# Kernel optimization log

Hardware: AMD Instinct MI355X
Metric: run time of the kernel (lower is better)

The kernel has to match this reference:

```python
import jax, jax.numpy as jnp
import numpy as np

SUPPORT = 10
NEIGHBOR_NUM = 20
DEGREE = 8
NEG_SLOPE = 0.2
EPS = 1e-12


def _norm(x, axis):
    n = jnp.linalg.norm(x, axis=axis, keepdims=True)
    return x / jnp.maximum(n, EPS)


def knn_index(v, k):
    # v: (b, n, 3) -> (b, n, k) indices of k nearest (self excluded)
    inner = jnp.einsum('bnd,bmd->bnm', v, v)
    quad = jnp.sum(v * v, axis=2)
    dist = quad[:, :, None] - 2.0 * inner + quad[:, None, :]
    _, idx = jax.lax.top_k(-dist, k + 1)  # smallest distances
    return idx[:, :, 1:]


def gather_nb(feat, idx):
    # feat (b,n,c), idx (b,n,k) -> (b,n,k,c)
    b = feat.shape[0]
    return feat[jnp.arange(b)[:, None, None], idx]


def nb_dir_norm(vertices, idx):
    nb = gather_nb(vertices, idx) - vertices[:, :, None, :]
    return _norm(nb, axis=-1)


def op3d(idx, vertices, directions, kernel_num):
    # Conv_surface: directions (3, support*kernel)
    ndn = nb_dir_norm(vertices, idx)                 # (b,n,k,3)
    sdn = _norm(directions, axis=0)
    theta = jax.nn.relu(jnp.einsum('bnkd,de->bnke', ndn, sdn))
    b, n, kk, _ = theta.shape
    theta = theta.reshape(b, n, kk, SUPPORT, kernel_num)
    return jnp.sum(jnp.max(theta, axis=2), axis=2)    # (b,n,kernel)


def opnd(idx, vertices, feat, w, bias, directions, out_ch):
    # Conv_layer: w (in,(s+1)*out), bias ((s+1)*out), directions (3, s*out)
    ndn = nb_dir_norm(vertices, idx)
    sdn = _norm(directions, axis=0)
    theta = jax.nn.relu(jnp.einsum('bnkd,de->bnke', ndn, sdn))  # (b,n,k,s*out)
    fo = feat @ w + bias                                        # (b,n,(s+1)*out)
    fc = fo[:, :, :out_ch]
    fs = gather_nb(fo[:, :, out_ch:], idx)                      # (b,n,k,s*out)
    b, n, kk, _ = theta.shape
    act = (theta * fs).reshape(b, n, kk, SUPPORT, out_ch)
    return fc + jnp.sum(jnp.max(act, axis=2), axis=2)


def tree_gcn(x, w_root, w_branch, w_l1, w_l2, bias, activation):
    # depth-0 upsampling TreeGCN: x (b,node,in) -> (b,node*DEGREE,out)
    b, node, in_f = x.shape
    root = x @ w_root                                           # (b,node,out)
    br = jax.nn.leaky_relu(jnp.einsum('bni,nij->bnj', x, w_branch), NEG_SLOPE)
    br = br.reshape(b, node * DEGREE, in_f)
    br = (br @ w_l1) @ w_l2                                     # (b,node*deg,out)
    out = jnp.repeat(root, DEGREE, axis=1) + br
    if activation:
        out = jax.nn.leaky_relu(out + jnp.tile(bias, (1, node, 1)), NEG_SLOPE)
    return out


def setup_inputs() -> dict:
    key = jax.random.key(0)
    ks = iter(jax.random.split(key, 32))
    r = lambda shape: (jax.random.normal(next(ks), shape, dtype=jnp.float32) * 0.1)
    inp = {
        'coase_points': jax.random.normal(next(ks), (2, 512, 3), dtype=jnp.float32),
        'd0': r((3, SUPPORT * 32)),
        'w1': r((32, (SUPPORT + 1) * 64)), 'b1': r(((SUPPORT + 1) * 64,)), 'dir1': r((3, SUPPORT * 64)),
        'd2': r((3, SUPPORT * 32)),
        'w3': r((32, (SUPPORT + 1) * 64)), 'b3': r(((SUPPORT + 1) * 64,)), 'dir3': r((3, SUPPORT * 64)),
        'w4': r((64, (SUPPORT + 1) * 64)), 'b4': r(((SUPPORT + 1) * 64,)), 'dir4': r((3, SUPPORT * 64)),
        'w5': r((64, (SUPPORT + 1) * 64)), 'b5': r(((SUPPORT + 1) * 64,)), 'dir5': r((3, SUPPORT * 64)),
        'root1': r((64, 3)), 'branch1': r((512, 64, DEGREE * 64)),
        'loop1a': r((64, 64 * SUPPORT)), 'loop1b': r((64 * SUPPORT, 3)), 'bias1': r((1, DEGREE, 3)),
        'root2': r((64, 3)), 'branch2': r((4096, 64, DEGREE * 64)),
        'loop2a': r((64, 64 * SUPPORT)), 'loop2b': r((64 * SUPPORT, 3)),
    }
    return inp


def reference(coase_points, d0, w1, b1, dir1, d2, w3, b3, dir3, w4, b4, dir4,
              w5, b5, dir5, root1, branch1, loop1a, loop1b, bias1,
              root2, branch2, loop2a, loop2b):
    idx = knn_index(coase_points, NEIGHBOR_NUM)
    fm0 = jax.nn.relu(op3d(idx, coase_points, d0, 32))  # dropout is identity in eval
    fm1 = jax.nn.relu(opnd(idx, coase_points, fm0, w1, b1, dir1, 64))
    pc1 = tree_gcn(fm1, root1, branch1, loop1a, loop1b, bias1, True)   # (b, 4096, 3)
    idx2 = knn_index(pc1, NEIGHBOR_NUM)
    fm2 = jax.nn.relu(op3d(idx2, pc1, d2, 32))
    fm3 = jax.nn.relu(opnd(idx2, pc1, fm2, w3, b3, dir3, 64))
    fm4 = jax.nn.relu(opnd(idx2, pc1, fm3, w4, b4, dir4, 64))
    fm5 = jax.nn.relu(opnd(idx2, pc1, fm4, w5, b5, dir5, 64))
    pc2 = tree_gcn(fm5, root2, branch2, loop2a, loop2b, None, False)   # (b, 32768, 3)
    return pc1, pc2
```

## Files before the change

kernel.cpp:

```cpp
#include <hip/hip_runtime.h>
#include <hip/hip_bf16.h>
#include <stdint.h>

#define SUPPORT 10
#define KNN 20
#define DEGREE 8

__global__ __launch_bounds__(256) void prep_kernel(
    const float* __restrict__ d0, const float* __restrict__ dir1,
    const float* __restrict__ d2, const float* __restrict__ dir3,
    const float* __restrict__ dir4, const float* __restrict__ dir5,
    float* __restrict__ sdn0, float* __restrict__ sdn1, float* __restrict__ sdn2,
    float* __restrict__ sdn3, float* __restrict__ sdn4, float* __restrict__ sdn5,
    const float* __restrict__ l1a, const float* __restrict__ l1b,
    const float* __restrict__ l2a, const float* __restrict__ l2b,
    float* __restrict__ wc1, float* __restrict__ wc2,
    const float* __restrict__ pts1,
    float* __restrict__ px1, float* __restrict__ py1, float* __restrict__ pz1) {
#pragma clang fp contract(off)
  if (blockIdx.x < 13) {
    int t = blockIdx.x * 256 + threadIdx.x;
    if (t >= 3200) return;
    const float* src; float* dst; int cols; int e;
    if (t < 320)       { src = d0;   dst = sdn0; cols = 320; e = t; }
    else if (t < 960)  { src = dir1; dst = sdn1; cols = 640; e = t - 320; }
    else if (t < 1280) { src = d2;   dst = sdn2; cols = 320; e = t - 960; }
    else if (t < 1920) { src = dir3; dst = sdn3; cols = 640; e = t - 1280; }
    else if (t < 2560) { src = dir4; dst = sdn4; cols = 640; e = t - 1920; }
    else               { src = dir5; dst = sdn5; cols = 640; e = t - 2560; }
    float a = src[e], b = src[cols + e], c = src[2 * cols + e];
    float nrm = sqrtf(a * a + b * b + c * c);
    nrm = fmaxf(nrm, 1e-12f);
    dst[e] = a / nrm; dst[cols + e] = b / nrm; dst[2 * cols + e] = c / nrm;
  } else if (blockIdx.x < 15) {
    int which = blockIdx.x - 13;
    int tt = threadIdx.x;
    if (tt >= 192) return;
    const float* A  = which ? l2a : l1a;
    const float* Bm = which ? l2b : l1b;
    float* out = which ? wc2 : wc1;
    int i = tt / 3, c = tt % 3;
    float s = 0.f;
    for (int k = 0; k < 640; ++k) s = fmaf(A[i * 640 + k], Bm[k * 3 + c], s);
    out[i * 3 + c] = s;
  } else {
    int t = (blockIdx.x - 15) * 256 + threadIdx.x;
    if (t >= 1024) return;
    px1[t] = pts1[t * 3];
    py1[t] = pts1[t * 3 + 1];
    pz1[t] = pts1[t * 3 + 2];
  }
}

__global__ __launch_bounds__(256) void soa2_kernel(const float* __restrict__ pc1,
                                                   float* __restrict__ px,
                                                   float* __restrict__ py,
                                                   float* __restrict__ pz) {
  int t = blockIdx.x * 256 + threadIdx.x;
  if (t >= 8192) return;
  px[t] = pc1[t * 3];
  py[t] = pc1[t * 3 + 1];
  pz[t] = pc1[t * 3 + 2];
}

template <int MPER, int WAVES>
__global__ __launch_bounds__(WAVES * 64) void knn_kernel(
    const float* __restrict__ px, const float* __restrict__ py,
    const float* __restrict__ pz, int N, int* __restrict__ idx_out) {
#pragma clang fp contract(off)
  extern __shared__ uint32_t kbuf[];
  int w = threadIdx.x >> 6, lane = threadIdx.x & 63;
  int g = blockIdx.x * WAVES + w;
  int b = g / N, n = g % N;
  volatile uint32_t* K = kbuf + (size_t)w * 64 * MPER;
  const float* PX = px + (size_t)b * N;
  const float* PY = py + (size_t)b * N;
  const float* PZ = pz + (size_t)b * N;

  float nx = PX[n], ny = PY[n], nz = PZ[n];
  float qn = nx * nx + ny * ny + nz * nz;

  unsigned long long mymin = ~0ull;
  for (int j = 0; j < MPER; ++j) {
    int m = j * 64 + lane;
    float mx = PX[m], my = PY[m], mz = PZ[m];
    float inner = nx * mx + ny * my + nz * mz;
    float qm = mx * mx + my * my + mz * mz;
    float d = (qn - 2.0f * inner) + qm;
    uint32_t u = __float_as_uint(d);
    u ^= (u & 0x80000000u) ? 0xFFFFFFFFu : 0x80000000u;
    K[lane * MPER + (j ^ (lane & (MPER - 1)))] = u;
    unsigned long long key = ((unsigned long long)u << 32) | (unsigned)m;
    mymin = key < mymin ? key : mymin;
  }
  for (int r = 0; r < 21; ++r) {
    unsigned long long best = mymin;
#pragma unroll
    for (int s = 1; s < 64; s <<= 1) {
      unsigned long long o = __shfl_xor(best, s, 64);
      best = o < best ? o : best;
    }
    unsigned m = (unsigned)best;
    if (r > 0 && lane == 0) idx_out[(size_t)g * KNN + (r - 1)] = (int)m;
    if (r == 20) break;
    int owner = m & 63, slot = m >> 6;
    if (lane == slot) K[owner * MPER + (slot ^ (owner & (MPER - 1)))] = 0xFFFFFFFFu;
    unsigned long long cand = ~0ull;
    if (lane < MPER) {
      uint32_t v = K[owner * MPER + (lane ^ (owner & (MPER - 1)))];
      cand = ((unsigned long long)v << 32) | (unsigned)(lane * 64 + owner);
    }
#pragma unroll
    for (int s = 1; s < 64; s <<= 1) {
      unsigned long long o = __shfl_xor(cand, s, 64);
      cand = o < cand ? o : cand;
    }
    if (lane == owner) mymin = cand;
  }
}

__global__ __launch_bounds__(256) void ndn_kernel(const float* __restrict__ pts,
                                                  const int* __restrict__ idx,
                                                  float* __restrict__ ndn, int N) {
#pragma clang fp contract(off)
  int t = blockIdx.x * 256 + threadIdx.x;
  int total = 2 * N * KNN;
  if (t >= total) return;
  int k = t % KNN, g = t / KNN;
  int b = g / N, n = g % N;
  int m = idx[(size_t)g * KNN + k];
  const float* pb = pts + (size_t)b * N * 3;
  float dx = pb[m * 3] - pb[n * 3];
  float dy = pb[m * 3 + 1] - pb[n * 3 + 1];
  float dz = pb[m * 3 + 2] - pb[n * 3 + 2];
  float nr = sqrtf(dx * dx + dy * dy + dz * dz);
  nr = fmaxf(nr, 1e-12f);
  ndn[(size_t)t * 3] = dx / nr; ndn[(size_t)t * 3 + 1] = dy / nr; ndn[(size_t)t * 3 + 2] = dz / nr;
}

__global__ __launch_bounds__(256) void op3d_kernel(const float* __restrict__ ndn,
                                                   const float* __restrict__ sdn,
                                                   float* __restrict__ out, int N) {
#pragma clang fp contract(off)
  int c = threadIdx.x & 31;
  int g = (blockIdx.x * 256 + threadIdx.x) >> 5;
  if (g >= 2 * N) return;
  const float* nd = ndn + (size_t)g * 60;
  float sv0[SUPPORT], sv1[SUPPORT], sv2[SUPPORT], mm[SUPPORT];
#pragma unroll
  for (int s = 0; s < SUPPORT; ++s) {
    sv0[s] = sdn[s * 32 + c];
    sv1[s] = sdn[320 + s * 32 + c];
    sv2[s] = sdn[640 + s * 32 + c];
    mm[s] = 0.f;
  }
  for (int k = 0; k < KNN; ++k) {
    float nx = nd[k * 3], ny = nd[k * 3 + 1], nz = nd[k * 3 + 2];
#pragma unroll
    for (int s = 0; s < SUPPORT; ++s) {
      float t = nx * sv0[s] + ny * sv1[s] + nz * sv2[s];
      mm[s] = fmaxf(mm[s], t);
    }
  }
  float acc = 0.f;
#pragma unroll
  for (int s = 0; s < SUPPORT; ++s) acc += mm[s];
  out[(size_t)g * 32 + c] = acc;
}

template <int K>
__global__ __launch_bounds__(256) void fo_kernel(const float* __restrict__ feat,
                                                 const float* __restrict__ wmat,
                                                 const float* __restrict__ bias,
                                                 float* __restrict__ fo, int N) {
  __shared__ float fL[8 * K];
  int t = threadIdx.x;
  int gbase = blockIdx.x * 8;
  for (int i = t; i < 8 * K; i += 256) fL[i] = feat[(size_t)gbase * K + i];
  __syncthreads();
  float a0[8], a1[8], a2[8];
#pragma unroll
  for (int gg = 0; gg < 8; ++gg) { a0[gg] = 0.f; a1[gg] = 0.f; a2[gg] = 0.f; }
  bool has3 = (t < 192);
  for (int i = 0; i < K; ++i) {
    float w0 = wmat[i * 704 + t];
    float w1 = wmat[i * 704 + t + 256];
    float w2 = has3 ? wmat[i * 704 + t + 512] : 0.f;
#pragma unroll
    for (int gg = 0; gg < 8; ++gg) {
      float f = fL[gg * K + i];
      a0[gg] = fmaf(f, w0, a0[gg]);
      a1[gg] = fmaf(f, w1, a1[gg]);
      a2[gg] = fmaf(f, w2, a2[gg]);
    }
  }
  float b0 = bias[t], b1 = bias[t + 256], b2 = has3 ? bias[t + 512] : 0.f;
#pragma unroll
  for (int gg = 0; gg < 8; ++gg) {
    size_t base = (size_t)(gbase + gg) * 704;
    fo[base + t] = a0[gg] + b0;
    fo[base + t + 256] = a1[gg] + b1;
    if (has3) fo[base + t + 512] = a2[gg] + b2;
  }
}

__global__ __launch_bounds__(256) void opnd_kernel(const float* __restrict__ ndn,
                                                   const int* __restrict__ idx,
                                                   const float* __restrict__ fo,
                                                   const float* __restrict__ sdn,
                                                   float* __restrict__ fm, int N) {
#pragma clang fp contract(off)
  __shared__ float ndL[4][64];
  __shared__ int offL[4][24];
  int nb = gridDim.x;
  int lb = (blockIdx.x & 7) * (nb >> 3) + (blockIdx.x >> 3);
  int w = threadIdx.x >> 6, lane = threadIdx.x & 63;
  int g = lb * 4 + w;
  if (lane < 60) ndL[w][lane] = ndn[(size_t)g * 60 + lane];
  if (lane < KNN) offL[w][lane] = ((g / N) * N + idx[(size_t)g * KNN + lane]) * 704 + 64;
  __syncthreads();
  const float* ndw = ndL[w];
  const int* offw = offL[w];
  float sv0[SUPPORT], sv1[SUPPORT], sv2[SUPPORT], mm[SUPPORT];
#pragma unroll
  for (int s = 0; s < SUPPORT; ++s) {
    sv0[s] = sdn[s * 64 + lane];
    sv1[s] = sdn[640 + s * 64 + lane];
    sv2[s] = sdn[1280 + s * 64 + lane];
    mm[s] = -__builtin_inff();
  }
  for (int k = 0; k < KNN; ++k) {
    float nx = ndw[k * 3], ny = ndw[k * 3 + 1], nz = ndw[k * 3 + 2];
    int off = offw[k];
#pragma unroll
    for (int s = 0; s < SUPPORT; ++s) {
      float t = fmaxf(nx * sv0[s] + ny * sv1[s] + nz * sv2[s], 0.f);
      float f = fo[(size_t)off + s * 64 + lane];
      mm[s] = fmaxf(mm[s], t * f);
    }
  }
  float acc = 0.f;
#pragma unroll
  for (int s = 0; s < SUPPORT; ++s) acc += mm[s];
  float fc = fo[(size_t)g * 704 + lane];
  float v = fc + acc;
  fm[(size_t)g * 64 + lane] = fmaxf(v, 0.f);
}

__global__ __launch_bounds__(256) void tree_exact_kernel(
    const float* __restrict__ x, const float* __restrict__ wroot,
    const float* __restrict__ wb, const float* __restrict__ l1,
    const float* __restrict__ l2, const float* __restrict__ bias,
    float* __restrict__ out, int node) {
#pragma clang fp contract(off)
  __shared__ float xL[2][64];
  __shared__ float brL[2][512];
  __shared__ float tL[16][640];
  __shared__ float rootv[2][3];
  int n = blockIdx.x, t = threadIdx.x;
  if (t < 128) xL[t >> 6][t & 63] = x[(size_t)(t >> 6) * node * 64 + (size_t)n * 64 + (t & 63)];
  __syncthreads();
  {
    const float* wrow = wb + (size_t)n * 64 * 512;
    int j0 = 2 * t;
    float a00 = 0.f, a01 = 0.f, a10 = 0.f, a11 = 0.f;
    for (int i = 0; i < 64; ++i) {
      float w0 = wrow[(size_t)i * 512 + j0];
      float w1 = wrow[(size_t)i * 512 + j0 + 1];
      float f0 = xL[0][i], f1 = xL[1][i];
      a00 = a00 + f0 * w0; a01 = a01 + f0 * w1;
      a10 = a10 + f1 * w0; a11 = a11 + f1 * w1;
    }
    brL[0][j0]     = a00 >= 0.f ? a00 : 0.2f * a00;
    brL[0][j0 + 1] = a01 >= 0.f ? a01 : 0.2f * a01;
    brL[1][j0]     = a10 >= 0.f ? a10 : 0.2f * a10;
    brL[1][j0 + 1] = a11 >= 0.f ? a11 : 0.2f * a11;
  }
  if (t < 6) {
    int b = t / 3, c = t % 3;
    float r = 0.f;
    for (int i = 0; i < 64; ++i) r = fmaf(xL[b][i], wroot[i * 3 + c], r);
    rootv[b][c] = r;
  }
  __syncthreads();
#pragma unroll 4
  for (int u = 0; u < 40; ++u) {
    int e = u * 256 + t;
    int p = e / 640, j = e % 640;
    const float* brow = brL[p >> 3] + (p & 7) * 64;
    float acc = 0.f;
    for (int i = 0; i < 64; ++i)
      acc = fmaf(brow[i], l1[i * 640 + j], acc);
    tL[p][j] = acc;
  }
  __syncthreads();
  if (t < 48) {
    int p = t / 3, c = t % 3, b = p >> 3, d = p & 7;
    float s = 0.f;
    for (int j = 0; j < 640; ++j) s = fmaf(tL[p][j], l2[j * 3 + c], s);
    float v = rootv[b][c] + s;
    v = v + bias[d * 3 + c];
    v = v >= 0.f ? v : 0.2f * v;
    out[((size_t)b * node * DEGREE + (size_t)n * DEGREE + d) * 3 + c] = v;
  }
}

__global__ __launch_bounds__(256) void tree_kernel(const float* __restrict__ x,
                                                   const float* __restrict__ wroot,
                                                   const float* __restrict__ wb,
                                                   const float* __restrict__ wc,
                                                   float* __restrict__ out,
                                                   int node) {
  __shared__ float xL[2][2][64];
  __shared__ float brL[2][2][512];
  int t = threadIdx.x;
  int n0 = blockIdx.x * 2;
  if (t < 256) {
    int which = t >> 6;
    int ns = which >> 1, bb = which & 1;
    xL[ns][bb][t & 63] = x[(size_t)bb * node * 64 + (size_t)(n0 + ns) * 64 + (t & 63)];
  }
  __syncthreads();
  int ns = t >> 7;
  int j0 = (t & 127) * 4;
  const float* wrow = wb + (size_t)(n0 + ns) * 64 * 512;
  float a0x = 0.f, a0y = 0.f, a0z = 0.f, a0w = 0.f;
  float a1x = 0.f, a1y = 0.f, a1z = 0.f, a1w = 0.f;
  for (int i = 0; i < 64; ++i) {
    float4 wv = *(const float4*)(wrow + (size_t)i * 512 + j0);
    float f0 = xL[ns][0][i], f1 = xL[ns][1][i];
    a0x += f0 * wv.x; a0y += f0 * wv.y; a0z += f0 * wv.z; a0w += f0 * wv.w;
    a1x += f1 * wv.x; a1y += f1 * wv.y; a1z += f1 * wv.z; a1w += f1 * wv.w;
  }
  brL[ns][0][j0]     = a0x >= 0.f ? a0x : 0.2f * a0x;
  brL[ns][0][j0 + 1] = a0y >= 0.f ? a0y : 0.2f * a0y;
  brL[ns][0][j0 + 2] = a0z >= 0.f ? a0z : 0.2f * a0z;
  brL[ns][0][j0 + 3] = a0w >= 0.f ? a0w : 0.2f * a0w;
  brL[ns][1][j0]     = a1x >= 0.f ? a1x : 0.2f * a1x;
  brL[ns][1][j0 + 1] = a1y >= 0.f ? a1y : 0.2f * a1y;
  brL[ns][1][j0 + 2] = a1z >= 0.f ? a1z : 0.2f * a1z;
  brL[ns][1][j0 + 3] = a1w >= 0.f ? a1w : 0.2f * a1w;
  __syncthreads();
  if (t < 96) {
    int nsub = t / 48, rem = t % 48;
    int b = rem / 24, r2 = rem % 24, d = r2 / 3, c = r2 % 3;
    float root = 0.f, brs = 0.f;
    for (int i = 0; i < 64; ++i) {
      root = fmaf(xL[nsub][b][i], wroot[i * 3 + c], root);
      brs  = fmaf(brL[nsub][b][d * 64 + i], wc[i * 3 + c], brs);
    }
    float v = root + brs;
    out[((size_t)b * node * DEGREE + (size_t)(n0 + nsub) * DEGREE + d) * 3 + c] = v;
  }
}

extern "C" void kernel_launch(void* const* d_in, const int* in_sizes, int n_in,
                              void* d_out, int out_size, void* d_ws, size_t ws_size,
                              hipStream_t stream) {
  const float* pts1    = (const float*)d_in[0];
  const float* d0      = (const float*)d_in[1];
  const float* w1      = (const float*)d_in[2];
  const float* b1      = (const float*)d_in[3];
  const float* dir1    = (const float*)d_in[4];
  const float* d2      = (const float*)d_in[5];
  const float* w3      = (const float*)d_in[6];
  const float* b3      = (const float*)d_in[7];
  const float* dir3    = (const float*)d_in[8];
  const float* w4      = (const float*)d_in[9];
  const float* b4      = (const float*)d_in[10];
  const float* dir4    = (const float*)d_in[11];
  const float* w5      = (const float*)d_in[12];
  const float* b5      = (const float*)d_in[13];
  const float* dir5    = (const float*)d_in[14];
  const float* root1   = (const float*)d_in[15];
  const float* branch1 = (const float*)d_in[16];
  const float* l1a     = (const float*)d_in[17];
  const float* l1b     = (const float*)d_in[18];
  const float* bias1   = (const float*)d_in[19];
  const float* root2   = (const float*)d_in[20];
  const float* branch2 = (const float*)d_in[21];
  const float* l2a     = (const float*)d_in[22];
  const float* l2b     = (const float*)d_in[23];

  float* ws = (float*)d_ws;
  size_t o = 0;
  float* sdn0 = ws + o; o += 960;
  float* sdn1 = ws + o; o += 1920;
  float* sdn2 = ws + o; o += 960;
  float* sdn3 = ws + o; o += 1920;
  float* sdn4 = ws + o; o += 1920;
  float* sdn5 = ws + o; o += 1920;
  float* wc1  = ws + o; o += 192;
  float* wc2  = ws + o; o += 192;
  float* px1  = ws + o; o += 1024;
  float* py1  = ws + o; o += 1024;
  float* pz1  = ws + o; o += 1024;
  float* px2  = ws + o; o += 8192;
  float* py2  = ws + o; o += 8192;
  float* pz2  = ws + o; o += 8192;
  int*   idxb = (int*)(ws + o); o += (size_t)2 * 4096 * KNN;
  float* ndnb = ws + o; o += (size_t)2 * 4096 * KNN * 3;
  float* fo   = ws + o; o += (size_t)2 * 4096 * 704;
  float* fmA  = ws + o; o += (size_t)2 * 4096 * 64;
  float* fmB  = ws + o; o += (size_t)2 * 4096 * 64;

  float* pc1 = (float*)d_out;
  float* pc2 = (float*)d_out + 2 * 4096 * 3;

  prep_kernel<<<19, 256, 0, stream>>>(d0, dir1, d2, dir3, dir4, dir5,
                                      sdn0, sdn1, sdn2, sdn3, sdn4, sdn5,
                                      l1a, l1b, l2a, l2b, wc1, wc2,
                                      pts1, px1, py1, pz1);

  knn_kernel<8, 4><<<2 * 512 / 4, 256, 4 * 64 * 8 * 4, stream>>>(px1, py1, pz1, 512, idxb);
  ndn_kernel<<<(2 * 512 * KNN + 255) / 256, 256, 0, stream>>>(pts1, idxb, ndnb, 512);
  op3d_kernel<<<2 * 512 * 32 / 256, 256, 0, stream>>>(ndnb, sdn0, fmA, 512);
  fo_kernel<32><<<2 * 512 / 8, 256, 0, stream>>>(fmA, w1, b1, fo, 512);
  opnd_kernel<<<2 * 512 / 4, 256, 0, stream>>>(ndnb, idxb, fo, sdn1, fmB, 512);
  tree_exact_kernel<<<512, 256, 0, stream>>>(fmB, root1, branch1, l1a, l1b,
                                             bias1, pc1, 512);

  soa2_kernel<<<32, 256, 0, stream>>>(pc1, px2, py2, pz2);
  knn_kernel<64, 2><<<2 * 4096 / 2, 128, 2 * 64 * 64 * 4, stream>>>(px2, py2, pz2, 4096, idxb);
  ndn_kernel<<<(2 * 4096 * KNN + 255) / 256, 256, 0, stream>>>(pc1, idxb, ndnb, 4096);
  op3d_kernel<<<2 * 4096 * 32 / 256, 256, 0, stream>>>(ndnb, sdn2, fmA, 4096);
  fo_kernel<32><<<2 * 4096 / 8, 256, 0, stream>>>(fmA, w3, b3, fo, 4096);
  opnd_kernel<<<2 * 4096 / 4, 256, 0, stream>>>(ndnb, idxb, fo, sdn3, fmB, 4096);
  fo_kernel<64><<<2 * 4096 / 8, 256, 0, stream>>>(fmB, w4, b4, fo, 4096);
  opnd_kernel<<<2 * 4096 / 4, 256, 0, stream>>>(ndnb, idxb, fo, sdn4, fmA, 4096);
  fo_kernel<64><<<2 * 4096 / 8, 256, 0, stream>>>(fmA, w5, b5, fo, 4096);
  opnd_kernel<<<2 * 4096 / 4, 256, 0, stream>>>(ndnb, idxb, fo, sdn5, fmB, 4096);
  tree_kernel<<<4096 / 2, 256, 0, stream>>>(fmB, root2, branch2, wc2, pc2, 4096);
}
```

Baseline: 655.3 us.

## Fuse neighbor-direction into kNN, op3d into fo, and SoA split into tree kernel

The kNN kernel now keeps the selected neighbor index in a per-lane register and, once selection ends, writes the indices and the normalized neighbor direction vectors directly. This removes the separate ndn kernel. op3d and the first feature matmul are merged into one kernel that keeps op3d output in shared memory. The first tree kernel also writes SoA coordinates, so the soa2 kernel is gone. The aim is fewer launches and less global round-tripping, at the cost of extra register and work load in the kNN and op3dfo kernels.

```diff
diff --git a/kernel.cpp b/kernel.cpp
--- a/kernel.cpp
+++ b/kernel.cpp
@@ -52,21 +52,11 @@
   }
 }
 
-__global__ __launch_bounds__(256) void soa2_kernel(const float* __restrict__ pc1,
-                                                   float* __restrict__ px,
-                                                   float* __restrict__ py,
-                                                   float* __restrict__ pz) {
-  int t = blockIdx.x * 256 + threadIdx.x;
-  if (t >= 8192) return;
-  px[t] = pc1[t * 3];
-  py[t] = pc1[t * 3 + 1];
-  pz[t] = pc1[t * 3 + 2];
-}
-
 template <int MPER, int WAVES>
 __global__ __launch_bounds__(WAVES * 64) void knn_kernel(
     const float* __restrict__ px, const float* __restrict__ py,
-    const float* __restrict__ pz, int N, int* __restrict__ idx_out) {
+    const float* __restrict__ pz, int N, int* __restrict__ idx_out,
+    float* __restrict__ ndn) {
 #pragma clang fp contract(off)
   extern __shared__ uint32_t kbuf[];
   int w = threadIdx.x >> 6, lane = threadIdx.x & 63;
@@ -93,6 +83,7 @@
     unsigned long long key = ((unsigned long long)u << 32) | (unsigned)m;
     mymin = key < mymin ? key : mymin;
   }
+  unsigned pick = 0;
   for (int r = 0; r < 21; ++r) {
     unsigned long long best = mymin;
 #pragma unroll
@@ -101,7 +92,7 @@
       best = o < best ? o : best;
     }
     unsigned m = (unsigned)best;
-    if (r > 0 && lane == 0) idx_out[(size_t)g * KNN + (r - 1)] = (int)m;
+    if (r > 0 && lane == r - 1) pick = m;
     if (r == 20) break;
     int owner = m & 63, slot = m >> 6;
     if (lane == slot) K[owner * MPER + (slot ^ (owner & (MPER - 1)))] = 0xFFFFFFFFu;
@@ -117,78 +108,100 @@
     }
     if (lane == owner) mymin = cand;
   }
-}
-
-__global__ __launch_bounds__(256) void ndn_kernel(const float* __restrict__ pts,
-                                                  const int* __restrict__ idx,
-                                                  float* __restrict__ ndn, int N) {
+  if (lane < KNN) {
+    idx_out[(size_t)g * KNN + lane] = (int)pick;
+    float mx = PX[pick], my = PY[pick], mz = PZ[pick];
+    float dx = mx - nx, dy = my - ny, dz = mz - nz;
+    float nr = sqrtf(dx * dx + dy * dy + dz * dz);
+    nr = fmaxf(nr, 1e-12f);
+    size_t base = (size_t)g * 60 + (size_t)lane * 3;
+    ndn[base] = dx / nr; ndn[base + 1] = dy / nr; ndn[base + 2] = dz / nr;
+  }
+}
+
+__global__ __launch_bounds__(256) void op3dfo_kernel(const float* __restrict__ ndn,
+                                                     const float* __restrict__ sdn,
+                                                     const float* __restrict__ wmat,
+                                                     const float* __restrict__ bias,
+                                                     float* __restrict__ fo, int N) {
 #pragma clang fp contract(off)
-  int t = blockIdx.x * 256 + threadIdx.x;
-  int total = 2 * N * KNN;
-  if (t >= total) return;
-  int k = t % KNN, g = t / KNN;
-  int b = g / N, n = g % N;
-  int m = idx[(size_t)g * KNN + k];
-  const float* pb = pts + (size_t)b * N * 3;
-  float dx = pb[m * 3] - pb[n * 3];
-  float dy = pb[m * 3 + 1] - pb[n * 3 + 1];
-  float dz = pb[m * 3 + 2] - pb[n * 3 + 2];
-  float nr = sqrtf(dx * dx + dy * dy + dz * dz);
-  nr = fmaxf(nr, 1e-12f);
-  ndn[(size_t)t * 3] = dx / nr; ndn[(size_t)t * 3 + 1] = dy / nr; ndn[(size_t)t * 3 + 2] = dz / nr;
-}
-
-__global__ __launch_bounds__(256) void op3d_kernel(const float* __restrict__ ndn,
-                                                   const float* __restrict__ sdn,
-                                                   float* __restrict__ out, int N) {
-#pragma clang fp contract(off)
-  int c = threadIdx.x & 31;
-  int g = (blockIdx.x * 256 + threadIdx.x) >> 5;
-  if (g >= 2 * N) return;
-  const float* nd = ndn + (size_t)g * 60;
-  float sv0[SUPPORT], sv1[SUPPORT], sv2[SUPPORT], mm[SUPPORT];
-#pragma unroll
-  for (int s = 0; s < SUPPORT; ++s) {
-    sv0[s] = sdn[s * 32 + c];
-    sv1[s] = sdn[320 + s * 32 + c];
-    sv2[s] = sdn[640 + s * 32 + c];
-    mm[s] = 0.f;
-  }
-  for (int k = 0; k < KNN; ++k) {
-    float nx = nd[k * 3], ny = nd[k * 3 + 1], nz = nd[k * 3 + 2];
+  __shared__ float ndL[8 * 60];
+  __shared__ float fL[8 * 32];
+  int t = threadIdx.x;
+  int gbase = blockIdx.x * 8;
+  for (int i = t; i < 8 * 60; i += 256) ndL[i] = ndn[(size_t)gbase * 60 + i];
+  __syncthreads();
+  {
+    int gg = t >> 5, c = t & 31;
+    const float* nd = ndL + gg * 60;
+    float sv0[SUPPORT], sv1[SUPPORT], sv2[SUPPORT], mm[SUPPORT];
 #pragma unroll
     for (int s = 0; s < SUPPORT; ++s) {
-      float t = nx * sv0[s] + ny * sv1[s] + nz * sv2[s];
-      mm[s] = fmaxf(mm[s], t);
-    }
-  }
-  float acc = 0.f;
-#pragma unroll
-  for (int s = 0; s < SUPPORT; ++s) acc += mm[s];
-  out[(size_t)g * 32 + c] = acc;
-}
-
-template <int K>
+      sv0[s] = sdn[s * 32 + c];
+      sv1[s] = sdn[320 + s * 32 + c];
+      sv2[s] = sdn[640 + s * 32 + c];
+      mm[s] = 0.f;
+    }
+    for (int k = 0; k < KNN; ++k) {
+      float nx = nd[k * 3], ny = nd[k * 3 + 1], nz = nd[k * 3 + 2];
+#pragma unroll
+      for (int s = 0; s < SUPPORT; ++s) {
+        float th = nx * sv0[s] + ny * sv1[s] + nz * sv2[s];
+        mm[s] = fmaxf(mm[s], th);
+      }
+    }
+    float acc = 0.f;
+#pragma unroll
+    for (int s = 0; s < SUPPORT; ++s) acc += mm[s];
+    fL[gg * 32 + c] = acc;
+  }
+  __syncthreads();
+  float a0[8], a1[8], a2[8];
+#pragma unroll
+  for (int gg = 0; gg < 8; ++gg) { a0[gg] = 0.f; a1[gg] = 0.f; a2[gg] = 0.f; }
+  bool has3 = (t < 192);
+  for (int i = 0; i < 32; ++i) {
+    float w0 = wmat[i * 704 + t];
+    float w1 = wmat[i * 704 + t + 256];
+    float w2 = has3 ? wmat[i * 704 + t + 512] : 0.f;
+#pragma unroll
+    for (int gg = 0; gg < 8; ++gg) {
+      float f = fL[gg * 32 + i];
+      a0[gg] = fmaf(f, w0, a0[gg]);
+      a1[gg] = fmaf(f, w1, a1[gg]);
+      a2[gg] = fmaf(f, w2, a2[gg]);
+    }
+  }
+  float b0 = bias[t], b1 = bias[t + 256], b2 = has3 ? bias[t + 512] : 0.f;
+#pragma unroll
+  for (int gg = 0; gg < 8; ++gg) {
+    size_t base = (size_t)(gbase + gg) * 704;
+    fo[base + t] = a0[gg] + b0;
+    fo[base + t + 256] = a1[gg] + b1;
+    if (has3) fo[base + t + 512] = a2[gg] + b2;
+  }
+}
+
 __global__ __launch_bounds__(256) void fo_kernel(const float* __restrict__ feat,
                                                  const float* __restrict__ wmat,
                                                  const float* __restrict__ bias,
                                                  float* __restrict__ fo, int N) {
-  __shared__ float fL[8 * K];
+  __shared__ float fL[8 * 64];
   int t = threadIdx.x;
   int gbase = blockIdx.x * 8;
-  for (int i = t; i < 8 * K; i += 256) fL[i] = feat[(size_t)gbase * K + i];
+  for (int i = t; i < 8 * 64; i += 256) fL[i] = feat[(size_t)gbase * 64 + i];
   __syncthreads();
   float a0[8], a1[8], a2[8];
 #pragma unroll
   for (int gg = 0; gg < 8; ++gg) { a0[gg] = 0.f; a1[gg] = 0.f; a2[gg] = 0.f; }
   bool has3 = (t < 192);
-  for (int i = 0; i < K; ++i) {
+  for (int i = 0; i < 64; ++i) {
     float w0 = wmat[i * 704 + t];
     float w1 = wmat[i * 704 + t + 256];
     float w2 = has3 ? wmat[i * 704 + t + 512] : 0.f;
 #pragma unroll
     for (int gg = 0; gg < 8; ++gg) {
-      float f = fL[gg * K + i];
+      float f = fL[gg * 64 + i];
       a0[gg] = fmaf(f, w0, a0[gg]);
       a1[gg] = fmaf(f, w1, a1[gg]);
       a2[gg] = fmaf(f, w2, a2[gg]);
@@ -251,7 +264,8 @@
     const float* __restrict__ x, const float* __restrict__ wroot,
     const float* __restrict__ wb, const float* __restrict__ l1,
     const float* __restrict__ l2, const float* __restrict__ bias,
-    float* __restrict__ out, int node) {
+    float* __restrict__ out, int node,
+    float* __restrict__ px2, float* __restrict__ py2, float* __restrict__ pz2) {
 #pragma clang fp contract(off)
   __shared__ float xL[2][64];
   __shared__ float brL[2][512];
@@ -302,6 +316,8 @@
     v = v + bias[d * 3 + c];
     v = v >= 0.f ? v : 0.2f * v;
     out[((size_t)b * node * DEGREE + (size_t)n * DEGREE + d) * 3 + c] = v;
+    int p2 = b * node * DEGREE + n * DEGREE + d;
+    if (c == 0) px2[p2] = v; else if (c == 1) py2[p2] = v; else pz2[p2] = v;
   }
 }
 
@@ -315,7 +331,7 @@
   __shared__ float brL[2][2][512];
   int t = threadIdx.x;
   int n0 = blockIdx.x * 2;
-  if (t < 256) {
+  {
     int which = t >> 6;
     int ns = which >> 1, bb = which & 1;
     xL[ns][bb][t & 63] = x[(size_t)bb * node * 64 + (size_t)(n0 + ns) * 64 + (t & 63)];
@@ -412,23 +428,18 @@
                                       l1a, l1b, l2a, l2b, wc1, wc2,
                                       pts1, px1, py1, pz1);
 
-  knn_kernel<8, 4><<<2 * 512 / 4, 256, 4 * 64 * 8 * 4, stream>>>(px1, py1, pz1, 512, idxb);
-  ndn_kernel<<<(2 * 512 * KNN + 255) / 256, 256, 0, stream>>>(pts1, idxb, ndnb, 512);
-  op3d_kernel<<<2 * 512 * 32 / 256, 256, 0, stream>>>(ndnb, sdn0, fmA, 512);
-  fo_kernel<32><<<2 * 512 / 8, 256, 0, stream>>>(fmA, w1, b1, fo, 512);
+  knn_kernel<8, 4><<<2 * 512 / 4, 256, 4 * 64 * 8 * 4, stream>>>(px1, py1, pz1, 512, idxb, ndnb);
+  op3dfo_kernel<<<2 * 512 / 8, 256, 0, stream>>>(ndnb, sdn0, w1, b1, fo, 512);
   opnd_kernel<<<2 * 512 / 4, 256, 0, stream>>>(ndnb, idxb, fo, sdn1, fmB, 512);
   tree_exact_kernel<<<512, 256, 0, stream>>>(fmB, root1, branch1, l1a, l1b,
-                                             bias1, pc1, 512);
-
-  soa2_kernel<<<32, 256, 0, stream>>>(pc1, px2, py2, pz2);
-  knn_kernel<64, 2><<<2 * 4096 / 2, 128, 2 * 64 * 64 * 4, stream>>>(px2, py2, pz2, 4096, idxb);
-  ndn_kernel<<<(2 * 4096 * KNN + 255) / 256, 256, 0, stream>>>(pc1, idxb, ndnb, 4096);
-  op3d_kernel<<<2 * 4096 * 32 / 256, 256, 0, stream>>>(ndnb, sdn2, fmA, 4096);
-  fo_kernel<32><<<2 * 4096 / 8, 256, 0, stream>>>(fmA, w3, b3, fo, 4096);
+                                             bias1, pc1, 512, px2, py2, pz2);
+
+  knn_kernel<64, 2><<<2 * 4096 / 2, 128, 2 * 64 * 64 * 4, stream>>>(px2, py2, pz2, 4096, idxb, ndnb);
+  op3dfo_kernel<<<2 * 4096 / 8, 256, 0, stream>>>(ndnb, sdn2, w3, b3, fo, 4096);
   opnd_kernel<<<2 * 4096 / 4, 256, 0, stream>>>(ndnb, idxb, fo, sdn3, fmB, 4096);
-  fo_kernel<64><<<2 * 4096 / 8, 256, 0, stream>>>(fmB, w4, b4, fo, 4096);
+  fo_kernel<<<2 * 4096 / 8, 256, 0, stream>>>(fmB, w4, b4, fo, 4096);
   opnd_kernel<<<2 * 4096 / 4, 256, 0, stream>>>(ndnb, idxb, fo, sdn4, fmA, 4096);
-  fo_kernel<64><<<2 * 4096 / 8, 256, 0, stream>>>(fmA, w5, b5, fo, 4096);
+  fo_kernel<<<2 * 4096 / 8, 256, 0, stream>>>(fmA, w5, b5, fo, 4096);
   opnd_kernel<<<2 * 4096 / 4, 256, 0, stream>>>(ndnb, idxb, fo, sdn5, fmB, 4096);
   tree_kernel<<<4096 / 2, 256, 0, stream>>>(fmB, root2, branch2, wc2, pc2, 4096);
 }
```

New measurement: 638.5 us. -2.6%, faster.
